# Performance work log

Hardware: AMD Instinct MI355X
Metric: run time of the kernel (lower is better)

Reference implementation:

```python
import jax, jax.numpy as jnp
import numpy as np

N_NODES = 100000
N_EDGES = 600000
D_IN = 128
D_OUT = 128
N_REL = 16
N_BASES = 8


def setup_inputs() -> dict:
    key = jax.random.key(0)
    ks = jax.random.split(key, 6)
    x = jax.random.normal(ks[0], (N_NODES, D_IN), dtype=jnp.float32)
    edge_index = jax.random.randint(ks[1], (2, N_EDGES), 0, N_NODES, dtype=jnp.int64)
    edge_type = jax.random.randint(ks[2], (N_EDGES,), 0, N_REL, dtype=jnp.int64)
    # xavier-uniform-ish init scales
    b_lim = float(np.sqrt(6.0 / (D_IN + D_OUT)))
    c_lim = float(np.sqrt(6.0 / (N_REL + N_BASES)))
    w_lim = float(np.sqrt(6.0 / (D_IN + D_OUT)))
    bases = jax.random.uniform(ks[3], (N_BASES, D_IN, D_OUT), jnp.float32, -b_lim, b_lim)
    coefficients = jax.random.uniform(ks[4], (N_REL, N_BASES), jnp.float32, -c_lim, c_lim)
    w_self = jax.random.uniform(ks[5], (D_OUT, D_IN), jnp.float32, -w_lim, w_lim)
    return {"x": x, "edge_index": edge_index, "edge_type": edge_type,
            "bases": bases, "coefficients": coefficients, "w_self": w_self}


def reference(x, edge_index, edge_type, bases, coefficients, w_self):
    # self loop: Linear(in, out, bias=False) -> x @ W^T
    out = x @ w_self.T  # [N, D_OUT]
    # relation weights from basis decomposition
    weights = jnp.einsum('rb,bio->rio', coefficients, bases)  # [R, D_IN, D_OUT]
    row, col = edge_index[0], edge_index[1]
    xc = x[col]  # [E, D_IN] gather of source features
    n_rel = weights.shape[0]
    msg = jnp.zeros((xc.shape[0], w_self.shape[0]), dtype=x.dtype)
    # fixed small loop over relations; masked accumulate matches per-relation grouped GEMM
    for r in range(n_rel):
        sel = (edge_type == r)[:, None]
        msg = msg + jnp.where(sel, xc @ weights[r], jnp.zeros((), x.dtype))
    # scatter-add messages to destination rows
    out = out.at[row].add(msg)
    return out
```

## Files before the change

### kernel.cpp

```cpp
#include <hip/hip_runtime.h>

#define NN 100000
#define NE 600000
#define ET (NE + NN)
#define D 128
#define NREL 16
#define SCANB 391
#define TPB 4
#define MAXTILES 10954
#define GEMMG ((MAXTILES + TPB - 1) / TPB)
#define WGRID 1088

typedef short short8 __attribute__((ext_vector_type(8)));
typedef float f32x4 __attribute__((ext_vector_type(4)));
typedef unsigned int u32x4 __attribute__((ext_vector_type(4)));

#define C0 0
#define O0 20
#define CU0 40
#define T0 60

#define WT_OFF   0
#define META_OFF 557056
#define DH_OFF   557568
#define DO_OFF   957568
#define DC_OFF   1357576
#define BS_OFF   1757576
#define SSRC_OFF 1759576
#define IDX_OFF  4559576
#define SDST_OFF 7359576
#define XB_OFF   10159576
#define MSG_OFF  35759576
#define NEED_XB  (XB_OFF + (size_t)NN * D * 2)
#define NEED_MSG (MSG_OFF + (size_t)ET * 128 * 2)

__device__ __forceinline__ unsigned short f2bf(float f) {
  unsigned u = __builtin_bit_cast(unsigned, f);
  u += 0x7fffu + ((u >> 16) & 1u);
  return (unsigned short)(u >> 16);
}

__global__ __launch_bounds__(256) void k_ph(const float* __restrict__ bases,
    const float* __restrict__ coef, const float* __restrict__ w_self,
    unsigned short* __restrict__ wT, const float* __restrict__ x,
    unsigned short* __restrict__ xb, const int* __restrict__ ei,
    const int* __restrict__ et, int* __restrict__ meta, int* __restrict__ dstHist,
    int xbf, int doMsg)
{
  int bx = blockIdx.x;
  int tid = threadIdx.x;
  if (bx < WGRID) {
    int idx = bx * 256 + tid;
    int r = idx >> 14;
    int t = idx & 16383;
    float v;
    if (r < 16) {
      int o = t >> 7, i = t & 127;
      float acc = 0.f;
      #pragma unroll
      for (int b = 0; b < 8; ++b)
        acc += coef[r * 8 + b] * bases[b * 16384 + i * 128 + o];
      v = acc;
    } else {
      v = w_self[t];
    }
    wT[idx] = f2bf(v);
    return;
  }
  int hb0 = WGRID + (xbf ? 12500 : 0);
  if (bx < hb0) {
    int i = (bx - WGRID) * 256 + tid;
    if (i >= NN * D / 4) return;
    f32x4 f = __builtin_nontemporal_load((const f32x4*)(x + (size_t)i * 4));
    unsigned short s0 = f2bf(f[0]), s1 = f2bf(f[1]), s2 = f2bf(f[2]), s3 = f2bf(f[3]);
    unsigned long long pk = (unsigned long long)s0 | ((unsigned long long)s1 << 16)
                          | ((unsigned long long)s2 << 32) | ((unsigned long long)s3 << 48);
    *(unsigned long long*)(xb + (size_t)i * 4) = pk;
    return;
  }
  __shared__ int h[16];
  int hb = bx - hb0;
  if (tid < 16) h[tid] = 0;
  __syncthreads();
  for (int e = hb * 256 + tid; e < NE; e += 256 * 256) {
    atomicAdd(&h[et[e]], 1);
    if (doMsg) atomicAdd(&dstHist[ei[e]], 1);
  }
  __syncthreads();
  if (tid < 16) atomicAdd(&meta[C0 + tid], h[tid]);
}

__global__ __launch_bounds__(256) void k_scan1(const int* __restrict__ dstHist,
    int* __restrict__ dstOff, int* __restrict__ blockSums)
{
  __shared__ int sh[256];
  int tid = threadIdx.x;
  int d = blockIdx.x * 256 + tid;
  int v = (d < NN) ? (dstHist[d] + 1) : 0;
  sh[tid] = v;
  __syncthreads();
  #pragma unroll
  for (int ofs = 1; ofs < 256; ofs <<= 1) {
    int t = (tid >= ofs) ? sh[tid - ofs] : 0;
    __syncthreads();
    sh[tid] += t;
    __syncthreads();
  }
  if (d < NN) dstOff[d] = sh[tid] - v;
  if (tid == 255) blockSums[blockIdx.x] = sh[tid];
}

__global__ __launch_bounds__(512) void k_scan2(int* __restrict__ blockSums, int* __restrict__ meta)
{
  __shared__ int sh[512];
  int tid = threadIdx.x;
  int v = (tid < SCANB) ? blockSums[tid] : 0;
  sh[tid] = v;
  __syncthreads();
  #pragma unroll
  for (int ofs = 1; ofs < 512; ofs <<= 1) {
    int t = (tid >= ofs) ? sh[tid - ofs] : 0;
    __syncthreads();
    sh[tid] += t;
    __syncthreads();
  }
  if (tid == 0) {
    meta[C0 + 16] = NN;
    int off = 0, toff = 0;
    for (int r = 0; r <= 16; ++r) {
      meta[O0 + r] = off;
      meta[CU0 + r] = off;
      meta[T0 + r] = toff;
      int c = meta[C0 + r];
      off += c;
      toff += (c + 63) >> 6;
    }
    meta[O0 + 17] = off;
    meta[T0 + 17] = toff;
  }
  if (tid < SCANB) blockSums[tid] = sh[tid] - v;
}

__global__ __launch_bounds__(256) void k_scan3(int* __restrict__ dstOff,
    const int* __restrict__ blockSums, int* __restrict__ dstCursor,
    int* __restrict__ sSrc, int* __restrict__ idx)
{
  int tid = threadIdx.x;
  int d = blockIdx.x * 256 + tid;
  int base = blockSums[blockIdx.x];
  if (d < NN) {
    int o = dstOff[d] + base;
    dstOff[d] = o;
    dstCursor[d] = o + 1;
    idx[o] = NE + d;
    sSrc[NE + d] = d;
  }
  if (d == NN) dstOff[NN] = ET;
}

__global__ __launch_bounds__(64) void k_meta(int* __restrict__ meta)
{
  if (threadIdx.x == 0) {
    meta[C0 + 16] = NN;
    int off = 0, toff = 0;
    for (int r = 0; r <= 16; ++r) {
      meta[O0 + r] = off;
      meta[CU0 + r] = off;
      meta[T0 + r] = toff;
      int c = meta[C0 + r];
      off += c;
      toff += (c + 63) >> 6;
    }
    meta[O0 + 17] = off;
    meta[T0 + 17] = toff;
  }
}

__global__ __launch_bounds__(256) void k_selfF(int* __restrict__ sSrc, int* __restrict__ sDst)
{
  int n = blockIdx.x * 256 + threadIdx.x;
  if (n < NN) { sSrc[NE + n] = n; sDst[NE + n] = n; }
}

__global__ __launch_bounds__(256) void k_scatter(const int* __restrict__ ei, const int* __restrict__ et,
    int* __restrict__ meta, int* __restrict__ sSrc, int* __restrict__ sDst,
    int* __restrict__ dstCursor, int* __restrict__ idx, int doMsg)
{
  __shared__ int h[16], base[16], lh[16];
  int tid = threadIdx.x;
  int start = blockIdx.x * 4096;
  int end = min(NE, start + 4096);
  if (tid < 16) { h[tid] = 0; lh[tid] = 0; }
  __syncthreads();
  for (int e = start + tid; e < end; e += 256)
    atomicAdd(&h[et[e]], 1);
  __syncthreads();
  if (tid < 16) base[tid] = atomicAdd(&meta[CU0 + tid], h[tid]);
  __syncthreads();
  for (int e = start + tid; e < end; e += 256) {
    int r = et[e];
    int row = ei[e];
    int pos = base[r] + atomicAdd(&lh[r], 1);
    sSrc[pos] = ei[NE + e];
    if (doMsg) idx[atomicAdd(&dstCursor[row], 1)] = pos;
    else sDst[pos] = row;
  }
}

__global__ __launch_bounds__(256) void k_gemm(const float* __restrict__ xf,
    const unsigned short* __restrict__ xb,
    const unsigned short* __restrict__ wT, const int* __restrict__ meta,
    const int* __restrict__ sSrc, const int* __restrict__ sDst,
    unsigned short* __restrict__ msg, float* __restrict__ out,
    int xbf, int msgmode)
{
  __shared__ short As[64 * 17 * 8];
  __shared__ short Es[64 * 136];
  __shared__ int Rows[64];
  __shared__ int Ms[80];

  int tid = threadIdx.x;
  if (tid < 80) Ms[tid] = meta[tid];
  __syncthreads();
  int ntiles = Ms[T0 + 17];
  int b0 = blockIdx.x * TPB;
  if (b0 >= ntiles) return;

  int lane = tid & 63, wave = tid >> 6;
  int q = lane >> 4, l15 = lane & 15;
  int m = tid >> 2, ug = tid & 3;

  int rprev = -1;
  short8 bfr[2][4];

  if (xbf && msgmode) {
    for (int ti = 0; ti < TPB; ++ti) {
      int b = b0 + ti;
      if (b >= ntiles) break;
      int r = 0;
      while (r < 16 && Ms[T0 + r + 1] <= b) ++r;
      int boff = Ms[O0 + r];
      int e0 = boff + (b - Ms[T0 + r]) * 64;
      int nr = min(64, boff + Ms[C0 + r] - e0);

      bool valid = m < nr;
      int src = sSrc[valid ? (e0 + m) : e0];
      const unsigned short* xr = xb + (size_t)src * 128;
      #pragma unroll
      for (int s = 0; s < 4; ++s) {
        int u = ug * 4 + s;
        short8 pk = (short8)(short)0;
        if (valid) pk = *(const short8*)(xr + u * 8);
        *(short8*)&As[(m * 17 + u) * 8] = pk;
      }
      __syncthreads();

      if (r != rprev) {
        const unsigned short* wr = wT + r * 16384;
        #pragma unroll
        for (int ns = 0; ns < 2; ++ns)
          #pragma unroll
          for (int kk = 0; kk < 4; ++kk)
            bfr[ns][kk] = *(const short8*)(wr + (wave * 32 + ns * 16 + l15) * 128 + kk * 32 + q * 8);
        rprev = r;
      }

      f32x4 acc[4][2];
      #pragma unroll
      for (int ms = 0; ms < 4; ++ms)
        #pragma unroll
        for (int ns = 0; ns < 2; ++ns)
          acc[ms][ns] = (f32x4){0.f, 0.f, 0.f, 0.f};
      #pragma unroll
      for (int kk = 0; kk < 4; ++kk) {
        short8 af[4];
        #pragma unroll
        for (int ms = 0; ms < 4; ++ms)
          af[ms] = *(const short8*)&As[((ms * 16 + l15) * 17 + kk * 4 + q) * 8];
        #pragma unroll
        for (int ms = 0; ms < 4; ++ms)
          #pragma unroll
          for (int ns = 0; ns < 2; ++ns)
            acc[ms][ns] = __builtin_amdgcn_mfma_f32_16x16x32_bf16(af[ms], bfr[ns][kk], acc[ms][ns], 0, 0, 0);
      }

      __syncthreads();
      #pragma unroll
      for (int ms = 0; ms < 4; ++ms)
        #pragma unroll
        for (int ns = 0; ns < 2; ++ns)
          #pragma unroll
          for (int reg = 0; reg < 4; ++reg)
            Es[(ms * 16 + q * 4 + reg) * 136 + wave * 32 + ns * 16 + l15] =
                (short)f2bf(acc[ms][ns][reg]);
      __syncthreads();

      #pragma unroll
      for (int i = 0; i < 4; ++i) {
        int row = wave * 16 + i * 4 + q;
        short8 v = *(const short8*)&Es[row * 136 + l15 * 8];
        if (row < nr)
          *(short8*)(msg + (size_t)(e0 + row) * 128 + l15 * 8) = v;
      }
      __syncthreads();
    }
    return;
  }

  for (int ti = 0; ti < TPB; ++ti) {
    int b = b0 + ti;
    if (b >= ntiles) break;
    int r = 0;
    while (r < 16 && Ms[T0 + r + 1] <= b) ++r;
    int boff = Ms[O0 + r];
    int e0 = boff + (b - Ms[T0 + r]) * 64;
    int nrows = min(64, boff + Ms[C0 + r] - e0);

    bool valid = m < nrows;
    int e = valid ? (e0 + m) : e0;
    int src = sSrc[e];
    if (ug == 0) Rows[m] = valid ? sDst[e] : 0;

    if (xbf) {
      const unsigned short* xr = xb + (size_t)src * 128;
      #pragma unroll
      for (int s = 0; s < 4; ++s) {
        int u = ug * 4 + s;
        short8 pk = (short8)(short)0;
        if (valid) pk = *(const short8*)(xr + u * 8);
        *(short8*)&As[(m * 17 + u) * 8] = pk;
      }
    } else {
      const float* xr = xf + (size_t)src * 128;
      #pragma unroll
      for (int s = 0; s < 4; ++s) {
        int u = ug * 4 + s;
        float4 f0 = make_float4(0.f, 0.f, 0.f, 0.f), f1 = f0;
        if (valid) {
          f0 = *(const float4*)(xr + u * 8);
          f1 = *(const float4*)(xr + u * 8 + 4);
        }
        short8 pk;
        pk[0] = (short)f2bf(f0.x); pk[1] = (short)f2bf(f0.y);
        pk[2] = (short)f2bf(f0.z); pk[3] = (short)f2bf(f0.w);
        pk[4] = (short)f2bf(f1.x); pk[5] = (short)f2bf(f1.y);
        pk[6] = (short)f2bf(f1.z); pk[7] = (short)f2bf(f1.w);
        *(short8*)&As[(m * 17 + u) * 8] = pk;
      }
    }
    __syncthreads();

    if (r != rprev) {
      const unsigned short* wr = wT + r * 16384;
      #pragma unroll
      for (int ns = 0; ns < 2; ++ns)
        #pragma unroll
        for (int kk = 0; kk < 4; ++kk)
          bfr[ns][kk] = *(const short8*)(wr + (wave * 32 + ns * 16 + l15) * 128 + kk * 32 + q * 8);
      rprev = r;
    }

    f32x4 acc[4][2];
    #pragma unroll
    for (int ms = 0; ms < 4; ++ms)
      #pragma unroll
      for (int ns = 0; ns < 2; ++ns)
        acc[ms][ns] = (f32x4){0.f, 0.f, 0.f, 0.f};
    #pragma unroll
    for (int kk = 0; kk < 4; ++kk) {
      short8 af[4];
      #pragma unroll
      for (int ms = 0; ms < 4; ++ms)
        af[ms] = *(const short8*)&As[((ms * 16 + l15) * 17 + kk * 4 + q) * 8];
      #pragma unroll
      for (int ms = 0; ms < 4; ++ms)
        #pragma unroll
        for (int ns = 0; ns < 2; ++ns)
          acc[ms][ns] = __builtin_amdgcn_mfma_f32_16x16x32_bf16(af[ms], bfr[ns][kk], acc[ms][ns], 0, 0, 0);
    }

    __syncthreads();
    #pragma unroll
    for (int ms = 0; ms < 4; ++ms)
      #pragma unroll
      for (int reg = 0; reg < 4; ++reg) {
        int mrow = ms * 16 + q * 4 + reg;
        if (mrow < nrows) {
          float* op = out + (size_t)Rows[mrow] * 128 + wave * 32 + l15;
          unsafeAtomicAdd(op, acc[ms][0][reg]);
          unsafeAtomicAdd(op + 16, acc[ms][1][reg]);
        }
      }
    __syncthreads();
  }
}

__global__ __launch_bounds__(256) void k_reduce(const unsigned short* __restrict__ msg,
    const int* __restrict__ dstOff, const int* __restrict__ idx,
    float* __restrict__ out)
{
  int d = blockIdx.x * 16 + (threadIdx.x >> 4);
  if (d >= NN) return;
  int sl = threadIdx.x & 15;
  int s = dstOff[d], e = dstOff[d + 1];
  const unsigned short* base = msg + (size_t)sl * 8;
  float a[8], bacc[8];
  #pragma unroll
  for (int i = 0; i < 8; ++i) { a[i] = 0.f; bacc[i] = 0.f; }
  int j = s;
  for (; j + 1 < e; j += 2) {
    size_t p0 = (size_t)idx[j] * 128;
    size_t p1 = (size_t)idx[j + 1] * 128;
    u32x4 v0 = *(const u32x4*)(base + p0);
    u32x4 v1 = *(const u32x4*)(base + p1);
    #pragma unroll
    for (int c = 0; c < 4; ++c) {
      a[2 * c]     += __builtin_bit_cast(float, v0[c] << 16);
      a[2 * c + 1] += __builtin_bit_cast(float, v0[c] & 0xffff0000u);
      bacc[2 * c]     += __builtin_bit_cast(float, v1[c] << 16);
      bacc[2 * c + 1] += __builtin_bit_cast(float, v1[c] & 0xffff0000u);
    }
  }
  if (j < e) {
    u32x4 v0 = *(const u32x4*)(base + (size_t)idx[j] * 128);
    #pragma unroll
    for (int c = 0; c < 4; ++c) {
      a[2 * c]     += __builtin_bit_cast(float, v0[c] << 16);
      a[2 * c + 1] += __builtin_bit_cast(float, v0[c] & 0xffff0000u);
    }
  }
  f32x4 w0, w1;
  w0[0] = a[0] + bacc[0]; w0[1] = a[1] + bacc[1]; w0[2] = a[2] + bacc[2]; w0[3] = a[3] + bacc[3];
  w1[0] = a[4] + bacc[4]; w1[1] = a[5] + bacc[5]; w1[2] = a[6] + bacc[6]; w1[3] = a[7] + bacc[7];
  float* op = out + (size_t)d * 128 + sl * 8;
  __builtin_nontemporal_store(w0, (f32x4*)op);
  __builtin_nontemporal_store(w1, (f32x4*)(op + 4));
}

extern "C" void kernel_launch(void* const* d_in, const int* in_sizes, int n_in,
                              void* d_out, int out_size, void* d_ws, size_t ws_size,
                              hipStream_t stream)
{
  const float* x      = (const float*)d_in[0];
  const int*   ei     = (const int*)d_in[1];
  const int*   et     = (const int*)d_in[2];
  const float* bases  = (const float*)d_in[3];
  const float* coef   = (const float*)d_in[4];
  const float* w_self = (const float*)d_in[5];
  float* out = (float*)d_out;
  char* ws = (char*)d_ws;
  unsigned short* wT = (unsigned short*)(ws + WT_OFF);
  int* meta      = (int*)(ws + META_OFF);
  int* dstHist   = (int*)(ws + DH_OFF);
  int* dstOff    = (int*)(ws + DO_OFF);
  int* dstCursor = (int*)(ws + DC_OFF);
  int* blockSums = (int*)(ws + BS_OFF);
  int* sSrc      = (int*)(ws + SSRC_OFF);
  int* idx       = (int*)(ws + IDX_OFF);
  int* sDst      = (int*)(ws + SDST_OFF);
  unsigned short* xb = (unsigned short*)(ws + XB_OFF);
  unsigned short* msg = (unsigned short*)(ws + MSG_OFF);

  const int msgmode = (ws_size >= NEED_MSG) ? 1 : 0;
  const int xbf = (msgmode || ws_size >= NEED_XB) ? 1 : 0;

  hipMemsetAsync(ws + META_OFF, 0, 512 + 400000, stream);
  k_ph<<<WGRID + (xbf ? 12500 : 0) + 256, 256, 0, stream>>>(
      bases, coef, w_self, wT, x, xb, ei, et, meta, dstHist, xbf, msgmode);
  if (msgmode) {
    k_scan1<<<SCANB, 256, 0, stream>>>(dstHist, dstOff, blockSums);
    k_scan2<<<1, 512, 0, stream>>>(blockSums, meta);
    k_scan3<<<SCANB, 256, 0, stream>>>(dstOff, blockSums, dstCursor, sSrc, idx);
  } else {
    k_meta<<<1, 64, 0, stream>>>(meta);
    k_selfF<<<SCANB, 256, 0, stream>>>(sSrc, sDst);
    hipMemsetAsync(d_out, 0, (size_t)NN * D * 4, stream);
  }
  k_scatter<<<(NE + 4095) / 4096, 256, 0, stream>>>(ei, et, meta, sSrc, sDst, dstCursor, idx, msgmode);
  k_gemm<<<GEMMG, 256, 0, stream>>>(x, xb, wT, meta, sSrc, sDst, msg, out, xbf, msgmode);
  if (msgmode)
    k_reduce<<<(NN + 15) / 16, 256, 0, stream>>>(msg, dstOff, idx, out);
}
```

Baseline: 329.7 us.

## Bin edges by relation and destination block to localize message scatter

Edges are now bucketed by (relation, destination>>10) instead of relation alone, so messages within each relation segment are ordered by destination range. The aim is better locality in the later reduce or scatter over destination rows. Tile metadata becomes a large prefix scan in a 1024-thread kernel, and a new k_tinfo kernel precomputes each tile's offset, row count and relation. The cost is more partially filled 64-row tiles, since 1568 bins each round up, which means extra GEMM work, plus an extra launch and larger shared histograms.

Result: slower. 345.3 us (+4.7%).

```diff
diff --git a/kernel.cpp b/kernel.cpp
--- a/kernel.cpp
+++ b/kernel.cpp
@@ -5,9 +5,12 @@
 #define ET (NE + NN)
 #define D 128
 #define NREL 16
+#define NB 98
+#define NBIN (NREL * NB)
+#define NBL (NBIN + 1)
 #define SCANB 391
 #define TPB 4
-#define MAXTILES 10954
+#define MAXTILES 12544
 #define GEMMG ((MAXTILES + TPB - 1) / TPB)
 #define WGRID 1088
 
@@ -16,21 +19,23 @@
 typedef unsigned int u32x4 __attribute__((ext_vector_type(4)));
 
 #define C0 0
-#define O0 20
-#define CU0 40
-#define T0 60
+#define O0 1570
+#define CU0 3140
+#define T0 4710
+#define META_BYTES 25600
 
 #define WT_OFF   0
 #define META_OFF 557056
-#define DH_OFF   557568
-#define DO_OFF   957568
-#define DC_OFF   1357576
-#define BS_OFF   1757576
-#define SSRC_OFF 1759576
-#define IDX_OFF  4559576
-#define SDST_OFF 7359576
-#define XB_OFF   10159576
-#define MSG_OFF  35759576
+#define DH_OFF   582656
+#define TI_OFF   582656
+#define DO_OFF   982656
+#define DC_OFF   1382664
+#define BS_OFF   1782664
+#define SSRC_OFF 1784712
+#define IDX_OFF  4584712
+#define SDST_OFF 7384712
+#define XB_OFF   10184712
+#define MSG_OFF  35784712
 #define NEED_XB  (XB_OFF + (size_t)NN * D * 2)
 #define NEED_MSG (MSG_OFF + (size_t)ET * 128 * 2)
 
@@ -78,16 +83,18 @@
     *(unsigned long long*)(xb + (size_t)i * 4) = pk;
     return;
   }
-  __shared__ int h[16];
+  __shared__ int h[NBIN];
   int hb = bx - hb0;
-  if (tid < 16) h[tid] = 0;
+  for (int i = tid; i < NBIN; i += 256) h[i] = 0;
   __syncthreads();
   for (int e = hb * 256 + tid; e < NE; e += 256 * 256) {
-    atomicAdd(&h[et[e]], 1);
-    if (doMsg) atomicAdd(&dstHist[ei[e]], 1);
-  }
-  __syncthreads();
-  if (tid < 16) atomicAdd(&meta[C0 + tid], h[tid]);
+    int dst = ei[e];
+    atomicAdd(&h[et[e] * NB + (dst >> 10)], 1);
+    if (doMsg) atomicAdd(&dstHist[dst], 1);
+  }
+  __syncthreads();
+  for (int i = tid; i < NBIN; i += 256)
+    if (h[i]) atomicAdd(&meta[C0 + i], h[i]);
 }
 
 __global__ __launch_bounds__(256) void k_scan1(const int* __restrict__ dstHist,
@@ -110,35 +117,62 @@
   if (tid == 255) blockSums[blockIdx.x] = sh[tid];
 }
 
-__global__ __launch_bounds__(512) void k_scan2(int* __restrict__ blockSums, int* __restrict__ meta)
-{
-  __shared__ int sh[512];
+__global__ __launch_bounds__(1024) void k_scan2(int* __restrict__ blockSums,
+    int* __restrict__ meta, int doMsg)
+{
+  __shared__ int sA[1024];
+  __shared__ int sB[1024];
   int tid = threadIdx.x;
-  int v = (tid < SCANB) ? blockSums[tid] : 0;
-  sh[tid] = v;
+
+  if (doMsg) {
+    int v = (tid < SCANB) ? blockSums[tid] : 0;
+    sA[tid] = v;
+    __syncthreads();
+    #pragma unroll
+    for (int ofs = 1; ofs < 1024; ofs <<= 1) {
+      int t = (tid >= ofs) ? sA[tid - ofs] : 0;
+      __syncthreads();
+      sA[tid] += t;
+      __syncthreads();
+    }
+    if (tid < SCANB) blockSums[tid] = sA[tid] - v;
+    __syncthreads();
+  }
+
+  int i0 = tid * 2, i1 = tid * 2 + 1;
+  int c0 = (i0 < NBIN) ? meta[C0 + i0] : ((i0 == NBIN) ? NN : 0);
+  int c1 = (i1 < NBIN) ? meta[C0 + i1] : ((i1 == NBIN) ? NN : 0);
+  int t0 = (c0 + 63) >> 6, t1 = (c1 + 63) >> 6;
+  sA[tid] = c0 + c1;
+  sB[tid] = t0 + t1;
   __syncthreads();
   #pragma unroll
-  for (int ofs = 1; ofs < 512; ofs <<= 1) {
-    int t = (tid >= ofs) ? sh[tid - ofs] : 0;
-    __syncthreads();
-    sh[tid] += t;
-    __syncthreads();
-  }
-  if (tid == 0) {
-    meta[C0 + 16] = NN;
-    int off = 0, toff = 0;
-    for (int r = 0; r <= 16; ++r) {
-      meta[O0 + r] = off;
-      meta[CU0 + r] = off;
-      meta[T0 + r] = toff;
-      int c = meta[C0 + r];
-      off += c;
-      toff += (c + 63) >> 6;
-    }
-    meta[O0 + 17] = off;
-    meta[T0 + 17] = toff;
-  }
-  if (tid < SCANB) blockSums[tid] = sh[tid] - v;
+  for (int ofs = 1; ofs < 1024; ofs <<= 1) {
+    int a = (tid >= ofs) ? sA[tid - ofs] : 0;
+    int b = (tid >= ofs) ? sB[tid - ofs] : 0;
+    __syncthreads();
+    sA[tid] += a;
+    sB[tid] += b;
+    __syncthreads();
+  }
+  int offEx = sA[tid] - (c0 + c1);
+  int tEx = sB[tid] - (t0 + t1);
+  if (i0 < NBL) {
+    meta[O0 + i0] = offEx;
+    meta[T0 + i0] = tEx;
+    if (i0 < NBIN) meta[CU0 + i0] = offEx;
+    meta[C0 + i0] = c0;
+  }
+  if (i1 < NBL) {
+    meta[O0 + i1] = offEx + c0;
+    meta[T0 + i1] = tEx + t0;
+    if (i1 < NBIN) meta[CU0 + i1] = offEx + c0;
+    meta[C0 + i1] = c1;
+  }
+  if (tid == 1023) {
+    meta[O0 + NBL] = sA[tid];
+    meta[T0 + NBL] = sB[tid];
+  }
 }
 
 __global__ __launch_bounds__(256) void k_scan3(int* __restrict__ dstOff,
@@ -158,49 +192,51 @@
   if (d == NN) dstOff[NN] = ET;
 }
 
-__global__ __launch_bounds__(64) void k_meta(int* __restrict__ meta)
-{
-  if (threadIdx.x == 0) {
-    meta[C0 + 16] = NN;
-    int off = 0, toff = 0;
-    for (int r = 0; r <= 16; ++r) {
-      meta[O0 + r] = off;
-      meta[CU0 + r] = off;
-      meta[T0 + r] = toff;
-      int c = meta[C0 + r];
-      off += c;
-      toff += (c + 63) >> 6;
-    }
-    meta[O0 + 17] = off;
-    meta[T0 + 17] = toff;
-  }
-}
-
 __global__ __launch_bounds__(256) void k_selfF(int* __restrict__ sSrc, int* __restrict__ sDst)
 {
   int n = blockIdx.x * 256 + threadIdx.x;
   if (n < NN) { sSrc[NE + n] = n; sDst[NE + n] = n; }
+}
+
+__global__ __launch_bounds__(256) void k_tinfo(const int* __restrict__ meta,
+    int4* __restrict__ tinfo)
+{
+  int t = blockIdx.x * 256 + threadIdx.x;
+  if (t >= MAXTILES) return;
+  int ntiles = meta[T0 + NBL];
+  if (t >= ntiles) { tinfo[t] = make_int4(0, 0, 0, 0); return; }
+  int lo = 0, hi = NBL;
+  while (lo < hi) {
+    int mid = (lo + hi + 1) >> 1;
+    if (meta[T0 + mid] <= t) lo = mid; else hi = mid - 1;
+  }
+  int bin = lo;
+  int e0 = meta[O0 + bin] + (t - meta[T0 + bin]) * 64;
+  int nr = min(64, meta[O0 + bin + 1] - e0);
+  int rel = (bin < NBIN) ? (bin / NB) : 16;
+  tinfo[t] = make_int4(e0, nr, rel, 0);
 }
 
 __global__ __launch_bounds__(256) void k_scatter(const int* __restrict__ ei, const int* __restrict__ et,
     int* __restrict__ meta, int* __restrict__ sSrc, int* __restrict__ sDst,
     int* __restrict__ dstCursor, int* __restrict__ idx, int doMsg)
 {
-  __shared__ int h[16], base[16], lh[16];
+  __shared__ int h[NBIN], base[NBIN], lh[NBIN];
   int tid = threadIdx.x;
   int start = blockIdx.x * 4096;
   int end = min(NE, start + 4096);
-  if (tid < 16) { h[tid] = 0; lh[tid] = 0; }
+  for (int i = tid; i < NBIN; i += 256) { h[i] = 0; lh[i] = 0; }
   __syncthreads();
   for (int e = start + tid; e < end; e += 256)
-    atomicAdd(&h[et[e]], 1);
-  __syncthreads();
-  if (tid < 16) base[tid] = atomicAdd(&meta[CU0 + tid], h[tid]);
+    atomicAdd(&h[et[e] * NB + (ei[e] >> 10)], 1);
+  __syncthreads();
+  for (int i = tid; i < NBIN; i += 256)
+    if (h[i]) base[i] = atomicAdd(&meta[CU0 + i], h[i]);
   __syncthreads();
   for (int e = start + tid; e < end; e += 256) {
-    int r = et[e];
     int row = ei[e];
-    int pos = base[r] + atomicAdd(&lh[r], 1);
+    int bin = et[e] * NB + (row >> 10);
+    int pos = base[bin] + atomicAdd(&lh[bin], 1);
     sSrc[pos] = ei[NE + e];
     if (doMsg) idx[atomicAdd(&dstCursor[row], 1)] = pos;
     else sDst[pos] = row;
@@ -211,18 +247,16 @@
     const unsigned short* __restrict__ xb,
     const unsigned short* __restrict__ wT, const int* __restrict__ meta,
     const int* __restrict__ sSrc, const int* __restrict__ sDst,
+    const int4* __restrict__ tinfo,
     unsigned short* __restrict__ msg, float* __restrict__ out,
     int xbf, int msgmode)
 {
   __shared__ short As[64 * 17 * 8];
   __shared__ short Es[64 * 136];
   __shared__ int Rows[64];
-  __shared__ int Ms[80];
 
   int tid = threadIdx.x;
-  if (tid < 80) Ms[tid] = meta[tid];
-  __syncthreads();
-  int ntiles = Ms[T0 + 17];
+  int ntiles = meta[T0 + NBL];
   int b0 = blockIdx.x * TPB;
   if (b0 >= ntiles) return;
 
@@ -237,11 +271,8 @@
     for (int ti = 0; ti < TPB; ++ti) {
       int b = b0 + ti;
       if (b >= ntiles) break;
-      int r = 0;
-      while (r < 16 && Ms[T0 + r + 1] <= b) ++r;
-      int boff = Ms[O0 + r];
-      int e0 = boff + (b - Ms[T0 + r]) * 64;
-      int nr = min(64, boff + Ms[C0 + r] - e0);
+      int4 ifo = tinfo[b];
+      int e0 = ifo.x, nr = ifo.y, r = ifo.z;
 
       bool valid = m < nr;
       int src = sSrc[valid ? (e0 + m) : e0];
@@ -310,11 +341,8 @@
   for (int ti = 0; ti < TPB; ++ti) {
     int b = b0 + ti;
     if (b >= ntiles) break;
-    int r = 0;
-    while (r < 16 && Ms[T0 + r + 1] <= b) ++r;
-    int boff = Ms[O0 + r];
-    int e0 = boff + (b - Ms[T0 + r]) * 64;
-    int nrows = min(64, boff + Ms[C0 + r] - e0);
+    int4 ifo = tinfo[b];
+    int e0 = ifo.x, nrows = ifo.y, r = ifo.z;
 
     bool valid = m < nrows;
     int e = valid ? (e0 + m) : e0;
@@ -452,6 +480,7 @@
   unsigned short* wT = (unsigned short*)(ws + WT_OFF);
   int* meta      = (int*)(ws + META_OFF);
   int* dstHist   = (int*)(ws + DH_OFF);
+  int4* tinfo    = (int4*)(ws + TI_OFF);
   int* dstOff    = (int*)(ws + DO_OFF);
   int* dstCursor = (int*)(ws + DC_OFF);
   int* blockSums = (int*)(ws + BS_OFF);
@@ -464,20 +493,21 @@
   const int msgmode = (ws_size >= NEED_MSG) ? 1 : 0;
   const int xbf = (msgmode || ws_size >= NEED_XB) ? 1 : 0;
 
-  hipMemsetAsync(ws + META_OFF, 0, 512 + 400000, stream);
+  hipMemsetAsync(ws + META_OFF, 0, META_BYTES + 400000, stream);
   k_ph<<<WGRID + (xbf ? 12500 : 0) + 256, 256, 0, stream>>>(
       bases, coef, w_self, wT, x, xb, ei, et, meta, dstHist, xbf, msgmode);
   if (msgmode) {
     k_scan1<<<SCANB, 256, 0, stream>>>(dstHist, dstOff, blockSums);
-    k_scan2<<<1, 512, 0, stream>>>(blockSums, meta);
+    k_scan2<<<1, 1024, 0, stream>>>(blockSums, meta, 1);
     k_scan3<<<SCANB, 256, 0, stream>>>(dstOff, blockSums, dstCursor, sSrc, idx);
   } else {
-    k_meta<<<1, 64, 0, stream>>>(meta);
+    k_scan2<<<1, 1024, 0, stream>>>(blockSums, meta, 0);
     k_selfF<<<SCANB, 256, 0, stream>>>(sSrc, sDst);
     hipMemsetAsync(d_out, 0, (size_t)NN * D * 4, stream);
   }
   k_scatter<<<(NE + 4095) / 4096, 256, 0, stream>>>(ei, et, meta, sSrc, sDst, dstCursor, idx, msgmode);
-  k_gemm<<<GEMMG, 256, 0, stream>>>(x, xb, wT, meta, sSrc, sDst, msg, out, xbf, msgmode);
+  k_tinfo<<<(MAXTILES + 255) / 256, 256, 0, stream>>>(meta, tinfo);
+  k_gemm<<<GEMMG, 256, 0, stream>>>(x, xb, wT, meta, sSrc, sDst, tinfo, msg, out, xbf, msgmode);
   if (msgmode)
     k_reduce<<<(NN + 15) / 16, 256, 0, stream>>>(msg, dstOff, idx, out);
 }
```
